# Kernel optimization log

Measured on AMD Instinct MI355X. Metric: run time of the kernel, lower is better.

Reference implementation:

```python
import jax, jax.numpy as jnp
import numpy as np

B, T, D = 64, 4096, 256
UNITS = 256

def setup_inputs() -> dict:
    key = jax.random.key(0)
    k0, k1, k2, k3 = jax.random.split(key, 4)
    lstm_output = jax.random.normal(k0, (B, T, D), dtype=jnp.float32)
    # Glorot-ish scaled dense weights (no bias per module)
    W1 = jax.random.normal(k1, (D, UNITS), dtype=jnp.float32) * (1.0 / np.sqrt(D))
    W2 = jax.random.normal(k2, (D, UNITS), dtype=jnp.float32) * (1.0 / np.sqrt(D))
    v = jax.random.normal(k3, (UNITS, 1), dtype=jnp.float32) * (1.0 / np.sqrt(UNITS))
    return {"lstm_output": lstm_output, "W1": W1, "W2": W2, "v": v}

def reference(lstm_output, W1, W2, v):
    # query/key: [B, T, units]
    query = jnp.einsum("btd,du->btu", lstm_output, W1)
    key = jnp.einsum("btd,du->btu", lstm_output, W2)
    # score: [B, T, 1]
    score = jnp.einsum("btu,uo->bto", jnp.tanh(query + key), v)
    # softmax over time axis (axis=1)
    attention_weights = jax.nn.softmax(score, axis=1)
    # context: [B, D]
    context_vector = jnp.sum(attention_weights * lstm_output, axis=1)
    return (context_vector, attention_weights)
```

## Files before the change

### kernel.cpp

```cpp
#include <hip/hip_runtime.h>
#include <math.h>

#define B 64
#define T 4096
#define D 256
#define U 256

typedef __attribute__((ext_vector_type(8)))  short s16x8;
typedef __attribute__((ext_vector_type(16))) float f32x16;

#define MT 32
#define SPB 16
#define NBLK ((B*T)/(MT*SPB))
#define LDAP 33

#define DPP_ADD(v, ctrl)                                                     \
  v += __int_as_float(__builtin_amdgcn_update_dpp(                           \
      0, __float_as_int(v), ctrl, 0xF, 0xF, true))

__device__ __forceinline__ void acc8(float* acc, float wr, uint4 h, uint4 l) {
  const unsigned* hw = (const unsigned*)&h;
  const unsigned* lw = (const unsigned*)&l;
#pragma unroll
  for (int jw = 0; jw < 4; ++jw) {
    const float ae = __uint_as_float(hw[jw] << 16) +
                     __uint_as_float(lw[jw] << 16);
    const float ao = __uint_as_float(hw[jw] & 0xffff0000u) +
                     __uint_as_float(lw[jw] & 0xffff0000u);
    acc[2 * jw]     = fmaf(wr, ae, acc[2 * jw]);
    acc[2 * jw + 1] = fmaf(wr, ao, acc[2 * jw + 1]);
  }
}

__global__ __launch_bounds__(512, 2) void scores_ctx_kernel(
    const float* __restrict__ A,
    const float* __restrict__ W1,
    const float* __restrict__ W2,
    const float* __restrict__ v,
    float* __restrict__ w_out,
    float* __restrict__ part,
    float* __restrict__ zpart)
{
  __shared__ uint4 AH[32 * LDAP];
  __shared__ uint4 AL[32 * LDAP];
  __shared__ float red[32][8];
  __shared__ float wbuf[32];

  const int tid  = threadIdx.x;
  const int lane = tid & 63;
  const int wv   = tid >> 6;
  const int l31  = lane & 31;
  const int half = lane >> 5;

  const int n = wv * 32 + l31;
  s16x8 Bh[16], Bl[16];
#pragma unroll
  for (int s = 0; s < 16; ++s) {
    s16x8 bh, bl;
#pragma unroll
    for (int j = 0; j < 8; ++j) {
      const int k = s * 16 + half * 8 + j;
      const float w = W1[k * 256 + n] + W2[k * 256 + n];
      const unsigned int uw = __float_as_uint(w);
      const float wl = w - __uint_as_float(uw & 0xffff0000u);
      bh[j] = (short)(uw >> 16);
      bl[j] = (short)(__float_as_uint(wl) >> 16);
    }
    Bh[s] = bh; Bl[s] = bl;
  }
  const float vv = v[n];

  const int sm  = tid >> 4;
  const int sc0 = tid & 15;

  const int k8c = tid >> 4;
  const int mlc = tid & 15;

  float acc[8] = {0.f, 0.f, 0.f, 0.f, 0.f, 0.f, 0.f, 0.f};
  float zacc = 0.f;

  const size_t row0 = (size_t)blockIdx.x * (MT * SPB);
  float4 rg[4];
  {
    const float4* src = (const float4*)(A + (row0 + sm) * 256);
#pragma unroll
    for (int i = 0; i < 4; ++i) rg[i] = src[sc0 + 16 * i];
  }

  for (int step = 0; step < SPB; ++step) {
    const size_t rowbase = row0 + (size_t)step * MT;

#pragma unroll
    for (int i = 0; i < 4; ++i) {
      const float4 a = rg[i];
      const int k  = 4 * (sc0 + 16 * i);
      const int k8 = k >> 3;
      const int off = (k >> 2) & 1;
      const unsigned int ux = __float_as_uint(a.x), uy = __float_as_uint(a.y);
      const unsigned int uz = __float_as_uint(a.z), uw = __float_as_uint(a.w);
      const uint2 hi2 = make_uint2((ux >> 16) | (uy & 0xffff0000u),
                                   (uz >> 16) | (uw & 0xffff0000u));
      const float lx = a.x - __uint_as_float(ux & 0xffff0000u);
      const float ly = a.y - __uint_as_float(uy & 0xffff0000u);
      const float lz = a.z - __uint_as_float(uz & 0xffff0000u);
      const float lw = a.w - __uint_as_float(uw & 0xffff0000u);
      const uint2 lo2 = make_uint2(
          (__float_as_uint(lx) >> 16) | (__float_as_uint(ly) & 0xffff0000u),
          (__float_as_uint(lz) >> 16) | (__float_as_uint(lw) & 0xffff0000u));
      ((uint2*)&AH[k8 * LDAP + sm])[off] = hi2;
      ((uint2*)&AL[k8 * LDAP + sm])[off] = lo2;
    }
    __syncthreads();

    if (step + 1 < SPB) {
      const float4* src = (const float4*)(A + (rowbase + MT + sm) * 256);
#pragma unroll
      for (int i = 0; i < 4; ++i) rg[i] = src[sc0 + 16 * i];
    }

    f32x16 a0 = {}, a1 = {}, a2 = {};
#pragma unroll
    for (int s = 0; s < 16; ++s) {
      const uint4 qh = AH[(2 * s + half) * LDAP + l31];
      const uint4 ql = AL[(2 * s + half) * LDAP + l31];
      const s16x8 ah = __builtin_bit_cast(s16x8, qh);
      const s16x8 al = __builtin_bit_cast(s16x8, ql);
      a0 = __builtin_amdgcn_mfma_f32_32x32x16_bf16(ah, Bh[s], a0, 0, 0, 0);
      a1 = __builtin_amdgcn_mfma_f32_32x32x16_bf16(ah, Bl[s], a1, 0, 0, 0);
      a2 = __builtin_amdgcn_mfma_f32_32x32x16_bf16(al, Bh[s], a2, 0, 0, 0);
    }

#pragma unroll
    for (int r = 0; r < 16; ++r) {
      const float x = a0[r] + a1[r] + a2[r];
      const float e = __expf(x + x);
      float p = (1.f - 2.f * __builtin_amdgcn_rcpf(e + 1.f)) * vv;
      DPP_ADD(p, 0xB1);
      DPP_ADD(p, 0x4E);
      DPP_ADD(p, 0x141);
      DPP_ADD(p, 0x140);
      p += __int_as_float(
          __builtin_amdgcn_ds_swizzle(__float_as_int(p), 0x401F));
      if (l31 == 0)
        red[(r & 3) + 8 * (r >> 2) + 4 * half][wv] = p;
    }
    __syncthreads();

    if (tid < 32) {
      const float4* rp = (const float4*)&red[tid][0];
      const float4 ra = rp[0], rb = rp[1];
      const float s =
          ra.x + ra.y + ra.z + ra.w + rb.x + rb.y + rb.z + rb.w;
      const float w = __expf(s);
      w_out[rowbase + tid] = w;
      wbuf[tid] = w;
      zacc += w;
    }
    __syncthreads();

    {
      const float w0 = wbuf[mlc];
      const float w1 = wbuf[mlc + 16];
      const uint4 h0 = AH[k8c * LDAP + mlc];
      const uint4 l0 = AL[k8c * LDAP + mlc];
      const uint4 h1 = AH[k8c * LDAP + mlc + 16];
      const uint4 l1 = AL[k8c * LDAP + mlc + 16];
      acc8(acc, w0, h0, l0);
      acc8(acc, w1, h1, l1);
    }
    __syncthreads();
  }

  float accsel = 0.f;
#pragma unroll
  for (int j = 0; j < 8; ++j) {
    float p = acc[j];
    DPP_ADD(p, 0xB1);
    DPP_ADD(p, 0x4E);
    DPP_ADD(p, 0x141);
    DPP_ADD(p, 0x140);
    if ((tid & 15) == j) accsel = p;
  }
  if ((tid & 15) < 8)
    part[blockIdx.x * 256 + k8c * 8 + (tid & 15)] = accsel;

  if (tid < 32) {
    float z = zacc;
    DPP_ADD(z, 0xB1);
    DPP_ADD(z, 0x4E);
    DPP_ADD(z, 0x141);
    DPP_ADD(z, 0x140);
    z += __int_as_float(
        __builtin_amdgcn_ds_swizzle(__float_as_int(z), 0x401F));
    if (tid == 0) zpart[blockIdx.x] = z;
  }
}

__global__ __launch_bounds__(1024) void finalize_kernel(
    const float* __restrict__ part,
    const float* __restrict__ zpart,
    float* __restrict__ attn,
    float* __restrict__ ctx)
{
  const int b = blockIdx.x;
  const int tid = threadIdx.x;
  __shared__ float shinv;
  if (tid == 0) {
    float z = 0.f;
#pragma unroll
    for (int c = 0; c < 8; ++c) z += zpart[b * 8 + c];
    shinv = 1.0f / z;
  }
  __syncthreads();
  const float iz = shinv;

  if (tid < D) {
    float s = 0.f;
#pragma unroll
    for (int c = 0; c < 8; ++c) s += part[(b * 8 + c) * D + tid];
    ctx[b * D + tid] = s * iz;
  }

  float4* row = (float4*)(attn + (long)b * T);
  float4 w4 = row[tid];
  w4.x *= iz; w4.y *= iz; w4.z *= iz; w4.w *= iz;
  row[tid] = w4;
}

extern "C" void kernel_launch(void* const* d_in, const int* in_sizes, int n_in,
                              void* d_out, int out_size, void* d_ws, size_t ws_size,
                              hipStream_t stream) {
    const float* lstm = (const float*)d_in[0];
    const float* W1   = (const float*)d_in[1];
    const float* W2   = (const float*)d_in[2];
    const float* v    = (const float*)d_in[3];

    float* out  = (float*)d_out;
    float* ctx  = out;
    float* attn = out + B * D;

    float* part  = (float*)d_ws;
    float* zpart = part + NBLK * D;

    scores_ctx_kernel<<<NBLK, 512, 0, stream>>>(lstm, W1, W2, v, attn, part, zpart);
    finalize_kernel<<<B, 1024, 0, stream>>>(part, zpart, attn, ctx);
}
```

Baseline: 414.5 us.

## Accumulate context from fp32 registers and merge split-bf16 MFMA accumulators

```diff
diff --git a/kernel.cpp b/kernel.cpp
--- a/kernel.cpp
+++ b/kernel.cpp
@@ -17,20 +17,6 @@
 #define DPP_ADD(v, ctrl)                                                     \
   v += __int_as_float(__builtin_amdgcn_update_dpp(                           \
       0, __float_as_int(v), ctrl, 0xF, 0xF, true))
-
-__device__ __forceinline__ void acc8(float* acc, float wr, uint4 h, uint4 l) {
-  const unsigned* hw = (const unsigned*)&h;
-  const unsigned* lw = (const unsigned*)&l;
-#pragma unroll
-  for (int jw = 0; jw < 4; ++jw) {
-    const float ae = __uint_as_float(hw[jw] << 16) +
-                     __uint_as_float(lw[jw] << 16);
-    const float ao = __uint_as_float(hw[jw] & 0xffff0000u) +
-                     __uint_as_float(lw[jw] & 0xffff0000u);
-    acc[2 * jw]     = fmaf(wr, ae, acc[2 * jw]);
-    acc[2 * jw + 1] = fmaf(wr, ao, acc[2 * jw + 1]);
-  }
-}
 
 __global__ __launch_bounds__(512, 2) void scores_ctx_kernel(
     const float* __restrict__ A,
@@ -44,7 +30,8 @@
   __shared__ uint4 AH[32 * LDAP];
   __shared__ uint4 AL[32 * LDAP];
   __shared__ float red[32][8];
-  __shared__ float wbuf[32];
+  __shared__ float wavebuf[8][16][16];
+  __shared__ float zred[8];
 
   const int tid  = threadIdx.x;
   const int lane = tid & 63;
@@ -73,10 +60,9 @@
   const int sm  = tid >> 4;
   const int sc0 = tid & 15;
 
-  const int k8c = tid >> 4;
-  const int mlc = tid & 15;
-
-  float acc[8] = {0.f, 0.f, 0.f, 0.f, 0.f, 0.f, 0.f, 0.f};
+  float acc[16];
+#pragma unroll
+  for (int q = 0; q < 16; ++q) acc[q] = 0.f;
   float zacc = 0.f;
 
   const size_t row0 = (size_t)blockIdx.x * (MT * SPB);
@@ -112,13 +98,17 @@
     }
     __syncthreads();
 
+    float4 rgc[4];
+#pragma unroll
+    for (int i = 0; i < 4; ++i) rgc[i] = rg[i];
+
     if (step + 1 < SPB) {
       const float4* src = (const float4*)(A + (rowbase + MT + sm) * 256);
 #pragma unroll
       for (int i = 0; i < 4; ++i) rg[i] = src[sc0 + 16 * i];
     }
 
-    f32x16 a0 = {}, a1 = {}, a2 = {};
+    f32x16 a0 = {}, a1 = {};
 #pragma unroll
     for (int s = 0; s < 16; ++s) {
       const uint4 qh = AH[(2 * s + half) * LDAP + l31];
@@ -127,12 +117,12 @@
       const s16x8 al = __builtin_bit_cast(s16x8, ql);
       a0 = __builtin_amdgcn_mfma_f32_32x32x16_bf16(ah, Bh[s], a0, 0, 0, 0);
       a1 = __builtin_amdgcn_mfma_f32_32x32x16_bf16(ah, Bl[s], a1, 0, 0, 0);
-      a2 = __builtin_amdgcn_mfma_f32_32x32x16_bf16(al, Bh[s], a2, 0, 0, 0);
+      a1 = __builtin_amdgcn_mfma_f32_32x32x16_bf16(al, Bh[s], a1, 0, 0, 0);
     }
 
 #pragma unroll
     for (int r = 0; r < 16; ++r) {
-      const float x = a0[r] + a1[r] + a2[r];
+      const float x = a0[r] + a1[r];
       const float e = __expf(x + x);
       float p = (1.f - 2.f * __builtin_amdgcn_rcpf(e + 1.f)) * vv;
       DPP_ADD(p, 0xB1);
@@ -146,53 +136,58 @@
     }
     __syncthreads();
 
-    if (tid < 32) {
-      const float4* rp = (const float4*)&red[tid][0];
+    {
+      const float4* rp = (const float4*)&red[sm][0];
       const float4 ra = rp[0], rb = rp[1];
-      const float s =
+      const float s8 =
           ra.x + ra.y + ra.z + ra.w + rb.x + rb.y + rb.z + rb.w;
-      const float w = __expf(s);
-      w_out[rowbase + tid] = w;
-      wbuf[tid] = w;
-      zacc += w;
-    }
-    __syncthreads();
-
-    {
-      const float w0 = wbuf[mlc];
-      const float w1 = wbuf[mlc + 16];
-      const uint4 h0 = AH[k8c * LDAP + mlc];
-      const uint4 l0 = AL[k8c * LDAP + mlc];
-      const uint4 h1 = AH[k8c * LDAP + mlc + 16];
-      const uint4 l1 = AL[k8c * LDAP + mlc + 16];
-      acc8(acc, w0, h0, l0);
-      acc8(acc, w1, h1, l1);
-    }
-    __syncthreads();
-  }
-
-  float accsel = 0.f;
-#pragma unroll
-  for (int j = 0; j < 8; ++j) {
-    float p = acc[j];
-    DPP_ADD(p, 0xB1);
-    DPP_ADD(p, 0x4E);
-    DPP_ADD(p, 0x141);
-    DPP_ADD(p, 0x140);
-    if ((tid & 15) == j) accsel = p;
-  }
-  if ((tid & 15) < 8)
-    part[blockIdx.x * 256 + k8c * 8 + (tid & 15)] = accsel;
-
-  if (tid < 32) {
+      const float w = __expf(s8);
+      if (sc0 == 0) {
+        w_out[rowbase + sm] = w;
+        zacc += w;
+      }
+#pragma unroll
+      for (int i = 0; i < 4; ++i) {
+        acc[4 * i + 0] = fmaf(w, rgc[i].x, acc[4 * i + 0]);
+        acc[4 * i + 1] = fmaf(w, rgc[i].y, acc[4 * i + 1]);
+        acc[4 * i + 2] = fmaf(w, rgc[i].z, acc[4 * i + 2]);
+        acc[4 * i + 3] = fmaf(w, rgc[i].w, acc[4 * i + 3]);
+      }
+    }
+  }
+
+#pragma unroll
+  for (int q = 0; q < 16; ++q) {
+    float p = acc[q];
+    p += __shfl_xor(p, 16);
+    p += __shfl_xor(p, 32);
+    acc[q] = p;
+  }
+  if (lane < 16) {
+#pragma unroll
+    for (int q = 0; q < 16; ++q) wavebuf[wv][lane][q] = acc[q];
+  }
+  {
     float z = zacc;
-    DPP_ADD(z, 0xB1);
-    DPP_ADD(z, 0x4E);
-    DPP_ADD(z, 0x141);
-    DPP_ADD(z, 0x140);
-    z += __int_as_float(
-        __builtin_amdgcn_ds_swizzle(__float_as_int(z), 0x401F));
-    if (tid == 0) zpart[blockIdx.x] = z;
+    z += __shfl_xor(z, 16);
+    z += __shfl_xor(z, 32);
+    if (lane == 0) zred[wv] = z;
+  }
+  __syncthreads();
+
+  if (tid < 256) {
+    const int sc = (tid & 63) >> 2;
+    const int q  = 4 * (tid >> 6) + (tid & 3);
+    float ssum = 0.f;
+#pragma unroll
+    for (int wvi = 0; wvi < 8; ++wvi) ssum += wavebuf[wvi][sc][q];
+    part[blockIdx.x * 256 + tid] = ssum;
+  }
+  if (tid == 0) {
+    float zz = 0.f;
+#pragma unroll
+    for (int i = 0; i < 8; ++i) zz += zred[i];
+    zpart[blockIdx.x] = zz;
   }
 }
 
```

Result: faster. 397.0 us (-4.2%).
